# Kernel tuning notes

Measured on AMD Instinct MI355X. Metric: run time of the kernel, lower is better.

The kernel has to match this reference:

```python
import jax, jax.numpy as jnp
import numpy as np
from math import comb

B = 1024                 # num_batch
NUM, NVAR, NUM_OBS = 100, 11, 10
T_FIN = 15.0
K_P = 20.0; K_D = 2.0 * np.sqrt(20.0); K_P_V = 20.0
A_OBS, B_OBS = 8.0, 4.2
RHO_V, RHO_PROJ, RHO_LANE, RHO_OBS, RHO_OFFSET, RHO_INEQ = 1.0, 1.0, 100.0, 100.0, 1.0, 100.0
V_MIN, V_MAX, A_MAX = 0.1, 30.0, 8.0
MAXITER = 20
LATENT, HID, INP_DIM, TRAJ_DIM = 2, 1024, 55, 200


def _bernstein():
    # degree-10 Bernstein polynomial basis on [0, T_FIN], sampled at NUM points
    n = NVAR - 1
    s = np.linspace(0.0, 1.0, NUM)
    bm = lambda m: np.stack([comb(m, k) * s**k * (1.0 - s)**(m - k) for k in range(m + 1)], 1)
    P, B9, B8 = bm(n), bm(n - 1), bm(n - 2)
    Z = np.zeros(NUM)
    Pdot = np.stack([(n / T_FIN) * ((B9[:, k - 1] if k >= 1 else Z) - (B9[:, k] if k <= n - 1 else Z)) for k in range(n + 1)], 1)
    Pddot = np.stack([(n * (n - 1) / T_FIN**2) * ((B8[:, k - 2] if k >= 2 else Z) - 2.0 * (B8[:, k - 1] if 1 <= k <= n - 1 else Z) + (B8[:, k] if k <= n - 2 else Z)) for k in range(n + 1)], 1)
    return tuple(jnp.asarray(a, jnp.float32) for a in (P, Pdot, Pddot))


def _forward(inp, initial_state_ego, traj_gt, y_ub, y_lb, eps,
             enc_w1, enc_b1, enc_w2, enc_b2, enc_wmu, enc_bmu, enc_wlv, enc_blv,
             dec_w1, dec_b1, dec_w2, dec_b2, dec_w3, dec_b3,
             P, Pdot, Pddot, inp_mean, inp_std):
    Bn = inp.shape[0]
    tot_time = jnp.linspace(0.0, T_FIN, NUM)

    # ---- cVAE encode / reparameterize / decode ----
    inp_n = (inp - inp_mean) / inp_std
    h = jax.nn.relu(jnp.concatenate([inp_n, traj_gt], 1) @ enc_w1 + enc_b1)
    h = jax.nn.relu(h @ enc_w2 + enc_b2)
    mu = h @ enc_wmu + enc_bmu
    logvar = h @ enc_wlv + enc_blv
    z = mu + jnp.exp(0.5 * logvar) * eps
    h = jax.nn.relu(jnp.concatenate([z, inp_n], 1) @ dec_w1 + dec_b1)
    h = jax.nn.relu(h @ dec_w2 + dec_b2)
    nn_out = h @ dec_w3 + dec_b3          # (B, 8): 4 v_des + 4 y_des setpoints

    # ---- constant constraint matrices ----
    A_eq_x = jnp.stack([P[0], Pdot[0], Pddot[0]])                 # (3, 11)
    A_eq_y = jnp.stack([P[0], Pdot[0], Pddot[0], Pdot[-1]])       # (4, 11)
    A_pd = Pddot - K_P * P - K_D * Pdot
    A_vd = Pddot - K_P_V * Pdot
    cost_smooth = Pddot.T @ Pddot
    I = jnp.eye(NVAR, dtype=P.dtype)

    def kkt_inv(cost, A_eq):
        m = A_eq.shape[0]
        M = jnp.block([[cost, A_eq.T], [A_eq, jnp.zeros((m, m), cost.dtype)]])
        return jnp.linalg.inv(M)

    # ---- boundary conditions ----
    zb = jnp.zeros((Bn,), inp.dtype)
    b_eq_x = jnp.stack([zb, initial_state_ego[:, 2], zb], 1)
    b_eq_y = jnp.stack([zb, initial_state_ego[:, 3], zb, zb], 1)

    # ---- QP layer 1 (behavioral layer) ----
    # sum_i A_vd_i^T A_vd_i over the 4 row-partitions == A_vd^T A_vd
    cost1_x = cost_smooth + RHO_V * (A_vd.T @ A_vd)
    cost1_y = cost_smooth + RHO_OFFSET * (A_pd.T @ A_pd)
    inv1_x = kkt_inv(cost1_x, A_eq_x)
    inv1_y = kkt_inv(cost1_y, A_eq_y)
    v_des = jnp.repeat(nn_out[:, 0:4], NUM // 4, axis=1)   # (B, 100) piecewise setpoints
    y_des = jnp.repeat(nn_out[:, 4:8], NUM // 4, axis=1)
    lincost_x1 = -RHO_V * ((-K_P_V * v_des) @ A_vd)
    lincost_y1 = -RHO_OFFSET * ((-K_P * y_des) @ A_pd)
    c_x_bar = (jnp.concatenate([-lincost_x1, b_eq_x], 1) @ inv1_x.T)[:, :NVAR]
    c_y_bar = (jnp.concatenate([-lincost_y1, b_eq_y], 1) @ inv1_y.T)[:, :NVAR]

    # ---- obstacle constant-velocity rollouts (obstacle-major, matches tile(P)) ----
    x_obs, y_obs = inp[:, 5::5], inp[:, 6::5]
    vx_obs, vy_obs = inp[:, 7::5], inp[:, 8::5]
    x_obs_traj = (x_obs[:, :, None] + vx_obs[:, :, None] * tot_time).reshape(Bn, NUM_OBS * NUM)
    y_obs_traj = (y_obs[:, :, None] + vy_obs[:, :, None] * tot_time).reshape(Bn, NUM_OBS * NUM)

    # ---- QP layer 2 (iterative ADMM-style projection) ----
    A_obs_m = jnp.tile(P, (NUM_OBS, 1))          # (1000, 11)
    A_lane = jnp.vstack([P, -P])                 # (200, 11)
    A_vel, A_acc = Pdot, Pddot
    cost2_x = RHO_PROJ * I + RHO_OBS * (A_obs_m.T @ A_obs_m) + RHO_INEQ * (A_acc.T @ A_acc) + RHO_INEQ * (A_vel.T @ A_vel)
    cost2_y = cost2_x + RHO_LANE * (A_lane.T @ A_lane)
    inv2_x = kkt_inv(cost2_x, A_eq_x)
    inv2_y = kkt_inv(cost2_y, A_eq_y)
    ones_num = jnp.ones((1, NUM), inp.dtype)
    b_lane = jnp.concatenate([y_ub[:, None] * ones_num, -y_lb[:, None] * ones_num], 1)  # (B, 200)

    def step(carry, _):
        primal, lx, ly = carry
        cx, cy = primal[:, :NVAR], primal[:, NVAR:]
        x, xdot, xddot = cx @ P.T, cx @ Pdot.T, cx @ Pddot.T
        y, ydot, yddot = cy @ P.T, cy @ Pdot.T, cy @ Pddot.T
        # obstacle polar decomposition
        wc = jnp.tile(x, (1, NUM_OBS)) - x_obs_traj
        ws = jnp.tile(y, (1, NUM_OBS)) - y_obs_traj
        a_o = jnp.arctan2(A_OBS * ws, B_OBS * wc)
        ca, sa = jnp.cos(a_o), jnp.sin(a_o)
        c1 = RHO_OBS * (A_OBS**2 * ca**2 + B_OBS**2 * sa**2)
        c2 = RHO_OBS * (A_OBS * wc * ca + B_OBS * ws * sa)
        d_o = jnp.maximum(1.0, c2 / c1)
        # velocity / acceleration polar decomposition with box clipping
        a_v = jnp.arctan2(ydot, xdot)
        cv, sv = jnp.cos(a_v), jnp.sin(a_v)
        d_v = jnp.clip(xdot * cv + ydot * sv, V_MIN, V_MAX)
        a_a = jnp.arctan2(yddot, xddot)
        caa, saa = jnp.cos(a_a), jnp.sin(a_a)
        d_a = jnp.clip(xddot * caa + yddot * saa, 0.0, A_MAX)
        # lane slack
        lane_proj = cy @ A_lane.T
        s_lane = jnp.maximum(0.0, b_lane - lane_proj)
        res_lane = lane_proj - b_lane + s_lane
        # residuals -> dual updates
        rxo = wc - A_OBS * d_o * ca
        ryo = ws - B_OBS * d_o * sa
        rvx, rvy = xdot - d_v * cv, ydot - d_v * sv
        rax, ray = xddot - d_a * caa, yddot - d_a * saa
        lx = lx - RHO_OBS * (rxo @ A_obs_m) - RHO_INEQ * (rax @ A_acc) - RHO_INEQ * (rvx @ A_vel)
        ly = ly - RHO_OBS * (ryo @ A_obs_m) - RHO_INEQ * (ray @ A_acc) - RHO_INEQ * (rvy @ A_vel) - RHO_LANE * (res_lane @ A_lane)
        # linear cost + batched KKT solve via precomputed inverse
        b_ox = x_obs_traj + A_OBS * d_o * ca
        b_oy = y_obs_traj + B_OBS * d_o * sa
        lin_x = -lx - RHO_PROJ * c_x_bar - RHO_OBS * (b_ox @ A_obs_m) - RHO_INEQ * ((d_a * caa) @ A_acc) - RHO_INEQ * ((d_v * cv) @ A_vel)
        lin_y = -ly - RHO_PROJ * c_y_bar - RHO_OBS * (b_oy @ A_obs_m) - RHO_INEQ * ((d_a * saa) @ A_acc) - RHO_INEQ * ((d_v * sv) @ A_vel) - RHO_LANE * ((b_lane - s_lane) @ A_lane)
        sx = (jnp.concatenate([-lin_x, b_eq_x], 1) @ inv2_x.T)[:, :NVAR]
        sy = (jnp.concatenate([-lin_y, b_eq_y], 1) @ inv2_y.T)[:, :NVAR]
        return (jnp.concatenate([sx, sy], 1), lx, ly), None

    primal0 = jnp.concatenate([c_x_bar, c_y_bar], 1)
    lam0 = jnp.zeros((Bn, NVAR), inp.dtype)
    (primal, _, _), _ = jax.lax.scan(step, (primal0, lam0, lam0), None, length=MAXITER)
    return primal  # (B, 2*NVAR) projected trajectory coefficients


def setup_inputs() -> dict:
    key = jax.random.key(0)
    ks = jax.random.split(key, 16)
    P, Pdot, Pddot = _bernstein()
    n = lambda k, sh, sc=1.0: sc * jax.random.normal(k, sh, jnp.float32)
    return {
        "inp": n(ks[0], (B, INP_DIM), 5.0),
        "initial_state_ego": jnp.concatenate([jnp.zeros((B, 2), jnp.float32), 10.0 + n(ks[1], (B, 2))], 1),
        "traj_gt": n(ks[2], (B, TRAJ_DIM)),
        "y_ub": jnp.full((B,), 3.5, jnp.float32),
        "y_lb": jnp.full((B,), -3.5, jnp.float32),
        "eps": n(ks[3], (B, LATENT)),
        "enc_w1": n(ks[4], (INP_DIM + TRAJ_DIM, HID), 0.05), "enc_b1": jnp.zeros((HID,), jnp.float32),
        "enc_w2": n(ks[5], (HID, HID), 0.03), "enc_b2": jnp.zeros((HID,), jnp.float32),
        "enc_wmu": n(ks[6], (HID, LATENT), 0.03), "enc_bmu": jnp.zeros((LATENT,), jnp.float32),
        "enc_wlv": n(ks[7], (HID, LATENT), 0.03), "enc_blv": jnp.zeros((LATENT,), jnp.float32),
        "dec_w1": n(ks[8], (LATENT + INP_DIM, HID), 0.05), "dec_b1": jnp.zeros((HID,), jnp.float32),
        "dec_w2": n(ks[9], (HID, HID), 0.03), "dec_b2": jnp.zeros((HID,), jnp.float32),
        "dec_w3": n(ks[10], (HID, 8), 0.03), "dec_b3": jnp.zeros((8,), jnp.float32),
        "P": P, "Pdot": Pdot, "Pddot": Pddot,
        "inp_mean": jnp.zeros((INP_DIM,), jnp.float32),
        "inp_std": jnp.ones((INP_DIM,), jnp.float32),
    }


def reference(inp, initial_state_ego, traj_gt, y_ub, y_lb, eps,
              enc_w1, enc_b1, enc_w2, enc_b2, enc_wmu, enc_bmu, enc_wlv, enc_blv,
              dec_w1, dec_b1, dec_w2, dec_b2, dec_w3, dec_b3,
              P, Pdot, Pddot, inp_mean, inp_std):
    return _forward(inp, initial_state_ego, traj_gt, y_ub, y_lb, eps,
                    enc_w1, enc_b1, enc_w2, enc_b2, enc_wmu, enc_bmu, enc_wlv, enc_blv,
                    dec_w1, dec_b1, dec_w2, dec_b2, dec_w3, dec_b3,
                    P, Pdot, Pddot, inp_mean, inp_std)
```

## Files before the change

kernel.cpp:

```cpp
#include <hip/hip_runtime.h>
#include <hip/hip_bf16.h>
#include <math.h>

#define BATCH   1024
#define NUMPT   100
#define NVAR    11
#define NOBS    10
#define HID     1024
#define INPD    55
#define TRAJD   200

#define T_FIN_C   15.0f
#define K_P_C     20.0f
#define K_D_C     8.944271909999159f
#define K_P_V_C   20.0f
#define A_OBS_C   8.0f
#define B_OBS_C   4.2f
#define AB_C      33.6f
#define ABSQ_C    1128.96f
#define RHO_V_C      1.0f
#define RHO_PROJ_C   1.0f
#define RHO_LANE_C   100.0f
#define RHO_OBS_C    100.0f
#define RHO_OFFSET_C 1.0f
#define RHO_INEQ_C   100.0f
#define V_MIN_C   0.1f
#define V_MAX_C   30.0f
#define A_MAX_C   8.0f
#define MAXIT     20

#define WS_INV1X  0
#define WS_INV1Y  256
#define WS_INV2X  512
#define WS_INV2Y  768
#define WS_SVD    1024
#define WS_SPD    1088
#define WS_QX     1152
#define WS_QY     1280
#define WS_R2X    1408
#define WS_R2Y    1536
#define WS_BIG    2048

typedef __bf16 bf16x8 __attribute__((ext_vector_type(8)));
typedef float  f32x4  __attribute__((ext_vector_type(4)));

__global__ __launch_bounds__(256) void setup_kernel(
    const float* __restrict__ Pg, const float* __restrict__ Pdg,
    const float* __restrict__ Pddg, float* __restrict__ ws,
    const float* __restrict__ inp, const float* __restrict__ traj,
    const float* __restrict__ mean, const float* __restrict__ stdv,
    __bf16* __restrict__ enc_in, __bf16* __restrict__ dec_in,
    const float* __restrict__ w1, const float* __restrict__ w2,
    const float* __restrict__ w3, const float* __restrict__ w4,
    __bf16* __restrict__ o1, __bf16* __restrict__ o2,
    __bf16* __restrict__ o3, __bf16* __restrict__ o4)
{
    __shared__ float sP[NUMPT*NVAR], sPd[NUMPT*NVAR], sPdd[NUMPT*NVAR];
    __shared__ float aug[15][31];
    __shared__ float fcol[15];
    __shared__ float sQ[121];
    __shared__ float sn[INPD];
    __shared__ float tile[64][65];
    __shared__ float s_pivinv;
    __shared__ int   s_pidx;
    const int tid = threadIdx.x, bid = blockIdx.x;

    if (bid >= 1028) {
        const int tb = bid - 1028;
        int wsel, kt, nt;
        if (tb < 64)       { wsel = 0; kt = tb >> 4;        nt = tb & 15; }
        else if (tb < 320) { wsel = 1; kt = (tb-64) >> 4;   nt = (tb-64) & 15; }
        else if (tb < 352) { wsel = 2; kt = (tb-320) >> 4;  nt = (tb-320) & 15; }
        else               { wsel = 3; kt = (tb-352) >> 4;  nt = (tb-352) & 15; }
        const float* W = (wsel==0) ? w1 : (wsel==1) ? w2 : (wsel==2) ? w3 : w4;
        __bf16* O      = (wsel==0) ? o1 : (wsel==1) ? o2 : (wsel==2) ? o3 : o4;
        const int K  = (wsel==0) ? 255 : (wsel==2) ? 57 : 1024;
        const int Kp = (wsel==0) ? 256 : (wsel==2) ? 128 : 1024;
        if (kt*64 >= Kp) return;
        const int k0 = kt*64, n0 = nt*64;
        const int rr = tid >> 6, c = tid & 63;
        #pragma unroll 4
        for (int it = 0; it < 16; ++it) {
            const int r = it*4 + rr;
            tile[r][c] = (k0 + r < K) ? W[(size_t)(k0 + r)*HID + n0 + c] : 0.0f;
        }
        __syncthreads();
        #pragma unroll 4
        for (int it = 0; it < 16; ++it) {
            const int r = it*4 + rr;
            O[(size_t)(n0 + r)*Kp + k0 + c] = (__bf16)tile[c][r];
        }
        return;
    }

    if (bid >= 4) {
        const int b = bid - 4;
        if (tid < INPD) {
            const float v = (inp[b*INPD + tid] - mean[tid]) / stdv[tid];
            sn[tid] = v;
            enc_in[b*256 + tid] = (__bf16)v;
        } else if (tid < 255) {
            enc_in[b*256 + tid] = (__bf16)traj[b*TRAJD + (tid - INPD)];
        } else {
            enc_in[b*256 + 255] = (__bf16)0.0f;
        }
        __syncthreads();
        if (tid >= 2 && tid < 128)
            dec_in[b*128 + tid] = (__bf16)((tid < 57) ? sn[tid - 2] : 0.0f);
        return;
    }

    for (int i = tid; i < NUMPT*NVAR; i += 256) {
        sP[i] = Pg[i]; sPd[i] = Pdg[i]; sPdd[i] = Pddg[i];
    }
    for (int i = tid; i < 15*31; i += 256) (&aug[0][0])[i] = 0.0f;
    __syncthreads();

    const int N = (bid == 0 || bid == 2) ? 14 : 15;

    if (tid < 121) {
        const int i = tid / 11, j = tid % 11;
        float s = 0.0f;
        if (bid == 0) {
            for (int t = 0; t < NUMPT; ++t) {
                float pdd_i = sPdd[t*NVAR+i], pdd_j = sPdd[t*NVAR+j];
                float av_i = pdd_i - K_P_V_C * sPd[t*NVAR+i];
                float av_j = pdd_j - K_P_V_C * sPd[t*NVAR+j];
                s += pdd_i*pdd_j + RHO_V_C * av_i*av_j;
            }
        } else if (bid == 1) {
            for (int t = 0; t < NUMPT; ++t) {
                float pdd_i = sPdd[t*NVAR+i], pdd_j = sPdd[t*NVAR+j];
                float ap_i = pdd_i - K_P_C*sP[t*NVAR+i] - K_D_C*sPd[t*NVAR+i];
                float ap_j = pdd_j - K_P_C*sP[t*NVAR+j] - K_D_C*sPd[t*NVAR+j];
                s += pdd_i*pdd_j + RHO_OFFSET_C * ap_i*ap_j;
            }
        } else {
            float obs_w = RHO_OBS_C * (float)NOBS;
            if (bid == 3) obs_w += RHO_LANE_C * 2.0f;
            for (int t = 0; t < NUMPT; ++t) {
                float p_i = sP[t*NVAR+i],   p_j = sP[t*NVAR+j];
                float pd_i = sPd[t*NVAR+i], pd_j = sPd[t*NVAR+j];
                float pdd_i = sPdd[t*NVAR+i], pdd_j = sPdd[t*NVAR+j];
                s += obs_w*p_i*p_j + RHO_INEQ_C*(pdd_i*pdd_j + pd_i*pd_j);
            }
            if (i == j) s += RHO_PROJ_C;
        }
        aug[i][j] = s;
    }
    if (tid < 11) {
        const int i = tid;
        float a0 = sP[i], a1 = sPd[i], a2 = sPdd[i];
        aug[i][11] = a0; aug[11][i] = a0;
        aug[i][12] = a1; aug[12][i] = a1;
        aug[i][13] = a2; aug[13][i] = a2;
        if (N == 15) { float a3 = sPd[99*NVAR + i]; aug[i][14] = a3; aug[14][i] = a3; }
    }
    if (tid < N) aug[tid][N + tid] = 1.0f;

    if (bid == 0 && tid < 44) {
        const int c = tid / 11, k = tid % 11;
        float sv = 0.0f, sp = 0.0f;
        for (int t = 25*c; t < 25*c + 25; ++t) {
            float p = sP[t*NVAR+k], pd = sPd[t*NVAR+k], pdd = sPdd[t*NVAR+k];
            sv += pdd - K_P_V_C * pd;
            sp += pdd - K_P_C * p - K_D_C * pd;
        }
        ws[WS_SVD + tid] = sv;
        ws[WS_SPD + tid] = sp;
    }
    __syncthreads();

    if ((bid == 2 || bid == 3) && tid < 121) {
        float v = aug[tid/11][tid%11];
        if (tid/11 == tid%11) v -= RHO_PROJ_C;
        sQ[tid] = v;
        ws[(bid == 2 ? WS_QX : WS_QY) + tid] = v;
    }

    for (int k = 0; k < N; ++k) {
        if (tid == 0) {
            int p = k; float best = fabsf(aug[k][k]);
            for (int i = k+1; i < N; ++i) {
                float v = fabsf(aug[i][k]);
                if (v > best) { best = v; p = i; }
            }
            s_pidx = p;
        }
        __syncthreads();
        const int p = s_pidx;
        if (p != k && tid < 2*N) {
            float tmp = aug[k][tid]; aug[k][tid] = aug[p][tid]; aug[p][tid] = tmp;
        }
        __syncthreads();
        if (tid == 0) s_pivinv = 1.0f / aug[k][k];
        __syncthreads();
        if (tid < 2*N) aug[k][tid] *= s_pivinv;
        __syncthreads();
        if (tid < N) fcol[tid] = (tid == k) ? 0.0f : aug[tid][k];
        __syncthreads();
        for (int idx = tid; idx < N*2*N; idx += 256) {
            const int i = idx / (2*N), j = idx % (2*N);
            if (i != k) aug[i][j] = fmaf(-fcol[i], aug[k][j], aug[i][j]);
        }
        __syncthreads();
    }

    float* dst = ws + (bid == 0 ? WS_INV1X : bid == 1 ? WS_INV1Y
                      : bid == 2 ? WS_INV2X : WS_INV2Y);
    for (int idx = tid; idx < N*N; idx += 256)
        dst[idx] = aug[idx / N][N + idx % N];
    __syncthreads();

    if ((bid == 2 || bid == 3) && tid < 121) {
        const int k = tid / 11, j = tid % 11;
        float a = 0.0f;
        #pragma unroll
        for (int m = 0; m < 11; ++m) a = fmaf(aug[k][N + m], sQ[m*11 + j], a);
        ws[(bid == 2 ? WS_R2X : WS_R2Y) + tid] = a;
    }
}

#define GEMM_CORE(A_, Wt_, Kp_, ...)                                          \
    __shared__ __bf16 As[2][32][136];                                         \
    __shared__ __bf16 Bs[2][64][136];                                         \
    const int lane = tid & 63, wv = tid >> 6;                                 \
    const int wm = (wv >> 1) * 16, wn = (wv & 1) * 32;                        \
    const int ln = lane & 15, q = lane >> 4;                                  \
    const int row0 = blockIdx.y * 32, col0 = blockIdx.x * 64;                 \
    const int r16 = tid >> 4, ch = (tid & 15) * 8;                            \
    f32x4 acc0 = (f32x4){0,0,0,0}, acc1 = (f32x4){0,0,0,0};                   \
    {                                                                         \
        bf16x8 va = *(const bf16x8*)&(A_)[(size_t)(row0 + r16)*(Kp_) + ch];   \
        bf16x8 vb = *(const bf16x8*)&(A_)[(size_t)(row0 + r16 + 16)*(Kp_) + ch]; \
        __VA_ARGS__                                                           \
        *(bf16x8*)&As[0][r16][ch] = va;                                       \
        *(bf16x8*)&As[0][r16 + 16][ch] = vb;                                  \
        _Pragma("unroll")                                                     \
        for (int p = 0; p < 4; ++p)                                           \
            *(bf16x8*)&Bs[0][r16 + 16*p][ch] =                                \
                *(const bf16x8*)&(Wt_)[(size_t)(col0 + r16 + 16*p)*(Kp_) + ch]; \
    }                                                                         \
    __syncthreads();                                                          \
    int cur = 0;                                                              \
    for (int k0 = 128; k0 < (Kp_); k0 += 128) {                               \
        const bf16x8 nva = *(const bf16x8*)&(A_)[(size_t)(row0 + r16)*(Kp_) + k0 + ch]; \
        const bf16x8 nvb = *(const bf16x8*)&(A_)[(size_t)(row0 + r16 + 16)*(Kp_) + k0 + ch]; \
        const bf16x8 nw0 = *(const bf16x8*)&(Wt_)[(size_t)(col0 + r16)*(Kp_) + k0 + ch]; \
        const bf16x8 nw1 = *(const bf16x8*)&(Wt_)[(size_t)(col0 + r16 + 16)*(Kp_) + k0 + ch]; \
        const bf16x8 nw2 = *(const bf16x8*)&(Wt_)[(size_t)(col0 + r16 + 32)*(Kp_) + k0 + ch]; \
        const bf16x8 nw3 = *(const bf16x8*)&(Wt_)[(size_t)(col0 + r16 + 48)*(Kp_) + k0 + ch]; \
        _Pragma("unroll")                                                     \
        for (int kc = 0; kc < 4; ++kc) {                                      \
            const bf16x8 a  = *(const bf16x8*)&As[cur][wm + ln][kc*32 + q*8]; \
            const bf16x8 b0 = *(const bf16x8*)&Bs[cur][wn + ln][kc*32 + q*8]; \
            const bf16x8 b1 = *(const bf16x8*)&Bs[cur][wn + 16 + ln][kc*32 + q*8]; \
            acc0 = __builtin_amdgcn_mfma_f32_16x16x32_bf16(a, b0, acc0, 0, 0, 0); \
            acc1 = __builtin_amdgcn_mfma_f32_16x16x32_bf16(a, b1, acc1, 0, 0, 0); \
        }                                                                     \
        const int nxt = cur ^ 1;                                              \
        *(bf16x8*)&As[nxt][r16][ch] = nva;                                    \
        *(bf16x8*)&As[nxt][r16 + 16][ch] = nvb;                               \
        *(bf16x8*)&Bs[nxt][r16][ch] = nw0;                                    \
        *(bf16x8*)&Bs[nxt][r16 + 16][ch] = nw1;                               \
        *(bf16x8*)&Bs[nxt][r16 + 32][ch] = nw2;                               \
        *(bf16x8*)&Bs[nxt][r16 + 48][ch] = nw3;                               \
        __syncthreads();                                                      \
        cur = nxt;                                                            \
    }                                                                         \
    _Pragma("unroll")                                                         \
    for (int kc = 0; kc < 4; ++kc) {                                          \
        const bf16x8 a  = *(const bf16x8*)&As[cur][wm + ln][kc*32 + q*8];     \
        const bf16x8 b0 = *(const bf16x8*)&Bs[cur][wn + ln][kc*32 + q*8];     \
        const bf16x8 b1 = *(const bf16x8*)&Bs[cur][wn + 16 + ln][kc*32 + q*8]; \
        acc0 = __builtin_amdgcn_mfma_f32_16x16x32_bf16(a, b0, acc0, 0, 0, 0); \
        acc1 = __builtin_amdgcn_mfma_f32_16x16x32_bf16(a, b1, acc1, 0, 0, 0); \
    }

#define GEMM_WRITE_RELU(C_)                                                   \
    _Pragma("unroll")                                                         \
    for (int ni = 0; ni < 2; ++ni) {                                          \
        const int col = col0 + wn + ni*16 + ln;                               \
        const float bv = bias[col];                                           \
        const f32x4 av = ni ? acc1 : acc0;                                    \
        _Pragma("unroll")                                                     \
        for (int r = 0; r < 4; ++r) {                                         \
            const int row = row0 + wm + q*4 + r;                              \
            (C_)[(size_t)row * HID + col] = (__bf16)fmaxf(av[r] + bv, 0.0f);  \
        }                                                                     \
    }

__global__ __launch_bounds__(256) void gemm_relu(
    const __bf16* __restrict__ A, const __bf16* __restrict__ Wt,
    const float* __restrict__ bias, __bf16* __restrict__ C, int Kp)
{
    const int tid = threadIdx.x;
    GEMM_CORE(A, Wt, Kp)
    GEMM_WRITE_RELU(C)
}

__global__ __launch_bounds__(256) void gemm_mulv(
    const __bf16* __restrict__ A, const __bf16* __restrict__ Wt,
    const float* __restrict__ bias,
    const float* __restrict__ wmu, const float* __restrict__ wlv,
    float* __restrict__ pmulv, int Kp)
{
    const int tid = threadIdx.x;
    GEMM_CORE(A, Wt, Kp)
    const int c0 = col0 + wn + ln;
    const int c1 = c0 + 16;
    const float b0v = bias[c0], b1v = bias[c1];
    const float wm00 = wmu[c0*2+0], wm01 = wmu[c0*2+1];
    const float wm10 = wmu[c1*2+0], wm11 = wmu[c1*2+1];
    const float wl00 = wlv[c0*2+0], wl01 = wlv[c0*2+1];
    const float wl10 = wlv[c1*2+0], wl11 = wlv[c1*2+1];
    float pr[4][4];
    #pragma unroll
    for (int r = 0; r < 4; ++r) {
        const float h0 = fmaxf(acc0[r] + b0v, 0.0f);
        const float h1 = fmaxf(acc1[r] + b1v, 0.0f);
        pr[r][0] = fmaf(h0, wm00, h1*wm10);
        pr[r][1] = fmaf(h0, wm01, h1*wm11);
        pr[r][2] = fmaf(h0, wl00, h1*wl10);
        pr[r][3] = fmaf(h0, wl01, h1*wl11);
    }
    #pragma unroll
    for (int m = 1; m <= 8; m <<= 1)
        #pragma unroll
        for (int r = 0; r < 4; ++r)
            #pragma unroll
            for (int j = 0; j < 4; ++j)
                pr[r][j] += __shfl_xor(pr[r][j], m);
    if (ln == 0) {
        const int part = blockIdx.x*2 + (wv & 1);
        #pragma unroll
        for (int r = 0; r < 4; ++r) {
            const int row = row0 + wm + q*4 + r;
            *(float4*)&pmulv[(size_t)row*128 + part*4] =
                make_float4(pr[r][0], pr[r][1], pr[r][2], pr[r][3]);
        }
    }
}

__global__ __launch_bounds__(256) void gemm_zfix(
    const __bf16* __restrict__ A, const __bf16* __restrict__ Wt,
    const float* __restrict__ bias, __bf16* __restrict__ C, int Kp,
    const float* __restrict__ pmulv, const float* __restrict__ bmu,
    const float* __restrict__ blv, const float* __restrict__ eps)
{
    __shared__ float zsh[32][2];
    const int tid = threadIdx.x;
    {
        const int row = tid >> 3, pg = tid & 7;
        const int ra = blockIdx.y*32 + row;
        float4 s = make_float4(0.0f, 0.0f, 0.0f, 0.0f);
        #pragma unroll
        for (int p = pg*4; p < pg*4 + 4; ++p) {
            const float4 qa = *(const float4*)&pmulv[(size_t)ra*128 + p*4];
            s.x += qa.x; s.y += qa.y; s.z += qa.z; s.w += qa.w;
        }
        #pragma unroll
        for (int m = 1; m <= 4; m <<= 1) {
            s.x += __shfl_down(s.x, m);
            s.y += __shfl_down(s.y, m);
            s.z += __shfl_down(s.z, m);
            s.w += __shfl_down(s.w, m);
        }
        if (pg == 0) {
            zsh[row][0] = fmaf(expf(0.5f*(s.z + blv[0])), eps[ra*2+0], s.x + bmu[0]);
            zsh[row][1] = fmaf(expf(0.5f*(s.w + blv[1])), eps[ra*2+1], s.y + bmu[1]);
        }
    }
    __syncthreads();
    GEMM_CORE(A, Wt, Kp,
        if (ch == 0) {
            va[0] = (__bf16)zsh[r16][0];
            va[1] = (__bf16)zsh[r16][1];
            vb[0] = (__bf16)zsh[r16 + 16][0];
            vb[1] = (__bf16)zsh[r16 + 16][1];
        }
    )
    GEMM_WRITE_RELU(C)
}

__global__ __launch_bounds__(256) void gemm_out8(
    const __bf16* __restrict__ A, const __bf16* __restrict__ Wt,
    const float* __restrict__ bias, const float* __restrict__ w3,
    float* __restrict__ pnn, int Kp)
{
    const int tid = threadIdx.x;
    GEMM_CORE(A, Wt, Kp)
    const int c0 = col0 + wn + ln;
    const int c1 = c0 + 16;
    const float b0v = bias[c0], b1v = bias[c1];
    float pr[4][8];
    #pragma unroll
    for (int r = 0; r < 4; ++r) {
        const float h0 = fmaxf(acc0[r] + b0v, 0.0f);
        const float h1 = fmaxf(acc1[r] + b1v, 0.0f);
        #pragma unroll
        for (int j = 0; j < 8; ++j)
            pr[r][j] = fmaf(h0, w3[c0*8 + j], h1*w3[c1*8 + j]);
    }
    #pragma unroll
    for (int m = 1; m <= 8; m <<= 1)
        #pragma unroll
        for (int r = 0; r < 4; ++r)
            #pragma unroll
            for (int j = 0; j < 8; ++j)
                pr[r][j] += __shfl_xor(pr[r][j], m);
    if (ln == 0) {
        const int part = blockIdx.x*2 + (wv & 1);
        #pragma unroll
        for (int r = 0; r < 4; ++r) {
            const int row = row0 + wm + q*4 + r;
            *(float4*)&pnn[(size_t)row*256 + part*8] =
                make_float4(pr[r][0], pr[r][1], pr[r][2], pr[r][3]);
            *(float4*)&pnn[(size_t)row*256 + part*8 + 4] =
                make_float4(pr[r][4], pr[r][5], pr[r][6], pr[r][7]);
        }
    }
}

#define DOT11(bb, a0, a1, a2) \
    fmaf(bb[0],a0.x, fmaf(bb[1],a0.y, fmaf(bb[2],a0.z, fmaf(bb[3],a0.w, \
    fmaf(bb[4],a1.x, fmaf(bb[5],a1.y, fmaf(bb[6],a1.z, fmaf(bb[7],a1.w, \
    fmaf(bb[8],a2.x, fmaf(bb[9],a2.y, bb[10]*a2.z))))))))))

__global__ __launch_bounds__(256) void solver_kernel(
    const float* __restrict__ pnn, const float* __restrict__ b3,
    const float* __restrict__ inp,
    const float* __restrict__ ise, const float* __restrict__ yub_p,
    const float* __restrict__ ylb_p,
    const float* __restrict__ Pg, const float* __restrict__ Pdg,
    const float* __restrict__ Pddg,
    const float* __restrict__ ws, float* __restrict__ out)
{
    __shared__ __align__(16) float sBcol[3][11][108];
    __shared__ float s_i2x[196], s_i2y[225], sR2x[121], sR2y[121];
    __shared__ __align__(16) float rows[7][104];
    __shared__ float dval[2][80];
    __shared__ __align__(16) float cxs[12], cys[12];
    __shared__ float wlin[24];
    __shared__ float obsS[4][10];
    __shared__ float nnS[8];

    const int tid = threadIdx.x;
    const int e = blockIdx.x;

    for (int i = tid; i < 3*11*108; i += 256) {
        const int mat = i / 1188, rem = i - mat*1188;
        const int k = rem / 108, t = rem - k*108;
        const float* G = (mat == 0) ? Pg : (mat == 1 ? Pdg : Pddg);
        sBcol[mat][k][t] = (t < NUMPT) ? G[t*NVAR + k] : 0.0f;
    }
    for (int i = tid; i < 196; i += 256) s_i2x[i] = ws[WS_INV2X + i];
    for (int i = tid; i < 225; i += 256) s_i2y[i] = ws[WS_INV2Y + i];
    for (int i = tid; i < 121; i += 256) { sR2x[i] = ws[WS_R2X + i]; sR2y[i] = ws[WS_R2Y + i]; }
    if (tid >= 112 && tid < 152) {
        const int i = tid - 112;
        obsS[i/10][i%10] = inp[e*INPD + 5 + (i/10) + 5*(i%10)];
    }
    if (tid >= 192) {
        const int l = tid - 192;
        const int j = l & 7, pg = l >> 3;
        float s = 0.0f;
        #pragma unroll
        for (int p = pg*4; p < pg*4 + 4; ++p)
            s += pnn[(size_t)e*256 + p*8 + j];
        s += __shfl_down(s, 8);
        s += __shfl_down(s, 16);
        s += __shfl_down(s, 32);
        if (pg == 0) nnS[j] = b3[j] + s;
    }
    if (tid >= 64 && tid < 92) {
        const int i = tid - 64;
        rows[i >> 2][100 + (i & 3)] = 0.0f;
    }
    if (tid == 92) cxs[11] = 0.0f;
    if (tid == 93) cys[11] = 0.0f;

    const bool isA = (tid < 200);
    const int tA = tid >> 1, hA2 = tid & 1;
    const bool isB = (tid < 154);
    const int hB = (tid >= 77) ? 1 : 0;
    const int dB = tid - 77*hB;
    const int rB = dB / 11, kB = dB - 11*rB;
    const int mB = (rB==1||rB==4) ? 2 : ((rB==2||rB==5) ? 1 : 0);
    const float* colp = &sBcol[mB][kB][hB*52];
    const float* rowp = &rows[rB][hB*52];

    float bP[NVAR], bQ[NVAR];
    if (isA) {
        const float* Qsrc = hA2 ? Pddg : Pdg;
        #pragma unroll
        for (int k = 0; k < NVAR; ++k) {
            bP[k] = Pg[tA*NVAR+k];
            bQ[k] = Qsrc[tA*NVAR+k];
        }
    }

    const float vx0 = ise[e*4 + 2], vy0 = ise[e*4 + 3];
    const float yub = yub_p[e], ylb = ylb_p[e];
    __syncthreads();

    const float DT = T_FIN_C / 99.0f;
    float xo[5], yo[5];
    if (isA) {
        const int ob0 = 5*hA2;
        #pragma unroll
        for (int o = 0; o < 5; ++o) {
            xo[o] = fmaf(obsS[2][ob0+o], tA*DT, obsS[0][ob0+o]);
            yo[o] = fmaf(obsS[3][ob0+o], tA*DT, obsS[1][ob0+o]);
        }
    }

    if (tid < 11) {
        float s = 0;
        #pragma unroll
        for (int c = 0; c < 4; ++c)
            s = fmaf(nnS[c], ws[WS_SVD + c*11 + tid], s);
        wlin[tid] = RHO_V_C * K_P_V_C * s;
    } else if (tid < 22) {
        const int k = tid - 11;
        float s = 0;
        #pragma unroll
        for (int c = 0; c < 4; ++c)
            s = fmaf(nnS[4 + c], ws[WS_SPD + c*11 + k], s);
        wlin[tid] = RHO_OFFSET_C * K_P_C * s;
    }
    __syncthreads();

    float lam = 0.0f, cb = 0.0f;
    if (tid < 11) {
        const int k = tid;
        float a = vx0 * ws[WS_INV1X + k*14 + 12];
        #pragma unroll
        for (int j = 0; j < NVAR; ++j)
            a = fmaf(-wlin[j], ws[WS_INV1X + k*14 + j], a);
        cb = a; cxs[k] = a;
    } else if (tid < 22) {
        const int k = tid - 11;
        float a = vy0 * ws[WS_INV1Y + k*15 + 12];
        #pragma unroll
        for (int j = 0; j < NVAR; ++j)
            a = fmaf(-wlin[11 + j], ws[WS_INV1Y + k*15 + j], a);
        cb = a; cys[k] = a;
    }
    __syncthreads();

    for (int it = 0; it < MAXIT; ++it) {
        if (isA) {
            const float4 x0 = *(const float4*)&cxs[0];
            const float4 x1 = *(const float4*)&cxs[4];
            const float4 x2 = *(const float4*)&cxs[8];
            const float4 y0 = *(const float4*)&cys[0];
            const float4 y1 = *(const float4*)&cys[4];
            const float4 y2 = *(const float4*)&cys[8];
            const float px = DOT11(bP, x0, x1, x2);
            const float py = DOT11(bP, y0, y1, y2);
            const float qx = DOT11(bQ, x0, x1, x2);
            const float qy = DOT11(bQ, y0, y1, y2);

            float srx = 0.0f, sry = 0.0f;
            #pragma unroll
            for (int o = 0; o < 5; ++o) {
                const float wc = px - xo[o], wsv = py - yo[o];
                const float aw = A_OBS_C * wsv, bw = B_OBS_C * wc;
                const float r2 = aw*aw + bw*bw;
                if (r2 > 0.0f) {
                    const float f = (r2 < ABSQ_C) ? (1.0f - AB_C * rsqrtf(r2)) : 0.0f;
                    srx = fmaf(wc, f, srx);
                    sry = fmaf(wsv, f, sry);
                } else {
                    srx -= A_OBS_C;
                }
            }
            const float mrx = srx + __shfl_xor(srx, 1);
            const float mry = sry + __shfl_xor(sry, 1);

            if (hA2 == 0) {
                rows[0][tA] = mrx;
                rows[3][tA] = mry;
                const float rv2 = qx*qx + qy*qy;
                float vxr, vyr;
                if (rv2 > 0.0f) {
                    const float ri = rsqrtf(rv2);
                    const float dv = fminf(fmaxf(rv2*ri, V_MIN_C), V_MAX_C);
                    const float f = 1.0f - dv*ri;
                    vxr = qx*f; vyr = qy*f;
                } else { vxr = -V_MIN_C; vyr = 0.0f; }
                rows[2][tA] = vxr;  rows[5][tA] = vyr;
                rows[6][tA] = fmaxf(0.0f, py - yub) - fmaxf(0.0f, ylb - py);
            } else {
                const float ra2 = qx*qx + qy*qy;
                float axr = 0.0f, ayr = 0.0f;
                if (ra2 > A_MAX_C*A_MAX_C) {
                    const float ri = rsqrtf(ra2);
                    const float f = 1.0f - A_MAX_C*ri;
                    axr = qx*f; ayr = qy*f;
                }
                rows[1][tA] = axr;  rows[4][tA] = ayr;
            }
        }
        __syncthreads();

        if (isB) {
            float s0 = 0.0f, s1 = 0.0f;
            #pragma unroll
            for (int i = 0; i < 13; ++i) {
                const float4 rr = *(const float4*)&rowp[i*4];
                const float4 cc = *(const float4*)&colp[i*4];
                s0 = fmaf(rr.x, cc.x, s0); s1 = fmaf(rr.y, cc.y, s1);
                s0 = fmaf(rr.z, cc.z, s0); s1 = fmaf(rr.w, cc.w, s1);
            }
            dval[hB][dB] = s0 + s1;
        }
        __syncthreads();

        if (tid < 22) {
            const int k = (tid < 11) ? tid : tid - 11;
            float u;
            if (tid < 11)
                u = RHO_OBS_C * ((dval[0][k]      + dval[1][k])
                               + (dval[0][11 + k] + dval[1][11 + k])
                               + (dval[0][22 + k] + dval[1][22 + k]));
            else
                u = RHO_OBS_C * ((dval[0][33 + k] + dval[1][33 + k])
                               + (dval[0][44 + k] + dval[1][44 + k])
                               + (dval[0][55 + k] + dval[1][55 + k])
                               + (dval[0][66 + k] + dval[1][66 + k]));
            wlin[tid] = 2.0f*u - lam - cb;
            lam -= u;
        }
        __builtin_amdgcn_wave_barrier();
        if (tid < 22) {
            const int k = (tid < 11) ? tid : tid - 11;
            if (tid < 11) {
                float a = vx0 * s_i2x[k*14 + 12];
                #pragma unroll
                for (int j = 0; j < NVAR; ++j) {
                    a = fmaf(-wlin[j], s_i2x[k*14 + j], a);
                    a = fmaf(sR2x[k*11 + j], cxs[j], a);
                }
                cxs[k] = a;
            } else {
                float a = vy0 * s_i2y[k*15 + 12];
                #pragma unroll
                for (int j = 0; j < NVAR; ++j) {
                    a = fmaf(-wlin[11 + j], s_i2y[k*15 + j], a);
                    a = fmaf(sR2y[k*11 + j], cys[j], a);
                }
                cys[k] = a;
            }
        }
        __syncthreads();
    }

    if (tid < NVAR) {
        out[e*22 + tid]      = cxs[tid];
        out[e*22 + 11 + tid] = cys[tid];
    }
}

extern "C" void kernel_launch(void* const* d_in, const int* in_sizes, int n_in,
                              void* d_out, int out_size, void* d_ws, size_t ws_size,
                              hipStream_t stream)
{
    (void)in_sizes; (void)n_in; (void)out_size; (void)ws_size;
    const float* inp    = (const float*)d_in[0];
    const float* ise    = (const float*)d_in[1];
    const float* traj   = (const float*)d_in[2];
    const float* yub    = (const float*)d_in[3];
    const float* ylb    = (const float*)d_in[4];
    const float* eps    = (const float*)d_in[5];
    const float* enc_w1 = (const float*)d_in[6];
    const float* enc_b1 = (const float*)d_in[7];
    const float* enc_w2 = (const float*)d_in[8];
    const float* enc_b2 = (const float*)d_in[9];
    const float* wmu    = (const float*)d_in[10];
    const float* bmu    = (const float*)d_in[11];
    const float* wlv    = (const float*)d_in[12];
    const float* blv    = (const float*)d_in[13];
    const float* dec_w1 = (const float*)d_in[14];
    const float* dec_b1 = (const float*)d_in[15];
    const float* dec_w2 = (const float*)d_in[16];
    const float* dec_b2 = (const float*)d_in[17];
    const float* dec_w3 = (const float*)d_in[18];
    const float* dec_b3 = (const float*)d_in[19];
    const float* P      = (const float*)d_in[20];
    const float* Pd     = (const float*)d_in[21];
    const float* Pdd    = (const float*)d_in[22];
    const float* mean   = (const float*)d_in[23];
    const float* stdv   = (const float*)d_in[24];

    float* ws    = (float*)d_ws;
    float* pmulv = ws + WS_BIG;
    float* pnn   = pmulv + (size_t)BATCH*128;
    __bf16* bfb  = (__bf16*)(pnn + (size_t)BATCH*256);
    __bf16* enc_in = bfb;
    __bf16* dec_in = enc_in + (size_t)BATCH*256;
    __bf16* hA     = dec_in + (size_t)BATCH*128;
    __bf16* wt1    = hA + (size_t)BATCH*HID;
    __bf16* wt2    = wt1 + (size_t)HID*256;
    __bf16* wt3    = wt2 + (size_t)HID*HID;
    __bf16* wt4    = wt3 + (size_t)HID*128;
    float* outf = (float*)d_out;

    setup_kernel<<<4 + 1024 + 608, 256, 0, stream>>>(
        P, Pd, Pdd, ws, inp, traj, mean, stdv, enc_in, dec_in,
        enc_w1, enc_w2, dec_w1, dec_w2, wt1, wt2, wt3, wt4);

    dim3 g(16, 32);
    gemm_relu<<<g, 256, 0, stream>>>(enc_in, wt1, enc_b1, hA, 256);
    gemm_mulv<<<g, 256, 0, stream>>>(hA, wt2, enc_b2, wmu, wlv, pmulv, 1024);
    gemm_zfix<<<g, 256, 0, stream>>>(dec_in, wt3, dec_b1, hA, 128,
                                     pmulv, bmu, blv, eps);
    gemm_out8<<<g, 256, 0, stream>>>(hA, wt4, dec_b2, dec_w3, pnn, 1024);
    solver_kernel<<<BATCH, 256, 0, stream>>>(pnn, dec_b3, inp, ise, yub, ylb,
                                             P, Pd, Pdd, ws, outf);
}
```

Before: 215.1 us.

## Retile MLP GEMMs to 64x64 output tiles with 512 threads and 64-wide K steps

Changes the shared GEMM core from 32x64 output tiles with 256 threads and 128-wide K chunks to 64x64 tiles with 8 waves and 64-wide K chunks. Each block now reuses every loaded weight row across twice as many activation rows, halving redundant weight traffic, and the grid shrinks from 512 to 256 blocks. The trade-off is fewer blocks to spread across CUs, twice as many barrier iterations along K, and less MFMA work between syncs. Epilogue partial-index math and the z-injection in the decoder GEMM are adjusted to the new wave layout.

```diff
diff --git a/kernel.cpp b/kernel.cpp
--- a/kernel.cpp
+++ b/kernel.cpp
@@ -222,36 +222,28 @@
 }
 
 #define GEMM_CORE(A_, Wt_, Kp_, ...)                                          \
-    __shared__ __bf16 As[2][32][136];                                         \
-    __shared__ __bf16 Bs[2][64][136];                                         \
+    __shared__ __bf16 As[2][64][72];                                          \
+    __shared__ __bf16 Bs[2][64][72];                                          \
     const int lane = tid & 63, wv = tid >> 6;                                 \
-    const int wm = (wv >> 1) * 16, wn = (wv & 1) * 32;                        \
+    const int wm = (wv & 3) * 16, wn = (wv >> 2) * 32;                        \
     const int ln = lane & 15, q = lane >> 4;                                  \
-    const int row0 = blockIdx.y * 32, col0 = blockIdx.x * 64;                 \
-    const int r16 = tid >> 4, ch = (tid & 15) * 8;                            \
+    const int row0 = blockIdx.y * 64, col0 = blockIdx.x * 64;                 \
+    const int lrow = tid >> 3, lc8 = (tid & 7) * 8;                           \
     f32x4 acc0 = (f32x4){0,0,0,0}, acc1 = (f32x4){0,0,0,0};                   \
     {                                                                         \
-        bf16x8 va = *(const bf16x8*)&(A_)[(size_t)(row0 + r16)*(Kp_) + ch];   \
-        bf16x8 vb = *(const bf16x8*)&(A_)[(size_t)(row0 + r16 + 16)*(Kp_) + ch]; \
+        bf16x8 va = *(const bf16x8*)&(A_)[(size_t)(row0 + lrow)*(Kp_) + lc8]; \
         __VA_ARGS__                                                           \
-        *(bf16x8*)&As[0][r16][ch] = va;                                       \
-        *(bf16x8*)&As[0][r16 + 16][ch] = vb;                                  \
-        _Pragma("unroll")                                                     \
-        for (int p = 0; p < 4; ++p)                                           \
-            *(bf16x8*)&Bs[0][r16 + 16*p][ch] =                                \
-                *(const bf16x8*)&(Wt_)[(size_t)(col0 + r16 + 16*p)*(Kp_) + ch]; \
+        *(bf16x8*)&As[0][lrow][lc8] = va;                                     \
+        *(bf16x8*)&Bs[0][lrow][lc8] =                                         \
+            *(const bf16x8*)&(Wt_)[(size_t)(col0 + lrow)*(Kp_) + lc8];        \
     }                                                                         \
     __syncthreads();                                                          \
     int cur = 0;                                                              \
-    for (int k0 = 128; k0 < (Kp_); k0 += 128) {                               \
-        const bf16x8 nva = *(const bf16x8*)&(A_)[(size_t)(row0 + r16)*(Kp_) + k0 + ch]; \
-        const bf16x8 nvb = *(const bf16x8*)&(A_)[(size_t)(row0 + r16 + 16)*(Kp_) + k0 + ch]; \
-        const bf16x8 nw0 = *(const bf16x8*)&(Wt_)[(size_t)(col0 + r16)*(Kp_) + k0 + ch]; \
-        const bf16x8 nw1 = *(const bf16x8*)&(Wt_)[(size_t)(col0 + r16 + 16)*(Kp_) + k0 + ch]; \
-        const bf16x8 nw2 = *(const bf16x8*)&(Wt_)[(size_t)(col0 + r16 + 32)*(Kp_) + k0 + ch]; \
-        const bf16x8 nw3 = *(const bf16x8*)&(Wt_)[(size_t)(col0 + r16 + 48)*(Kp_) + k0 + ch]; \
+    for (int k0 = 64; k0 < (Kp_); k0 += 64) {                                 \
+        const bf16x8 nva = *(const bf16x8*)&(A_)[(size_t)(row0 + lrow)*(Kp_) + k0 + lc8]; \
+        const bf16x8 nwb = *(const bf16x8*)&(Wt_)[(size_t)(col0 + lrow)*(Kp_) + k0 + lc8]; \
         _Pragma("unroll")                                                     \
-        for (int kc = 0; kc < 4; ++kc) {                                      \
+        for (int kc = 0; kc < 2; ++kc) {                                      \
             const bf16x8 a  = *(const bf16x8*)&As[cur][wm + ln][kc*32 + q*8]; \
             const bf16x8 b0 = *(const bf16x8*)&Bs[cur][wn + ln][kc*32 + q*8]; \
             const bf16x8 b1 = *(const bf16x8*)&Bs[cur][wn + 16 + ln][kc*32 + q*8]; \
@@ -259,17 +251,13 @@
             acc1 = __builtin_amdgcn_mfma_f32_16x16x32_bf16(a, b1, acc1, 0, 0, 0); \
         }                                                                     \
         const int nxt = cur ^ 1;                                              \
-        *(bf16x8*)&As[nxt][r16][ch] = nva;                                    \
-        *(bf16x8*)&As[nxt][r16 + 16][ch] = nvb;                               \
-        *(bf16x8*)&Bs[nxt][r16][ch] = nw0;                                    \
-        *(bf16x8*)&Bs[nxt][r16 + 16][ch] = nw1;                               \
-        *(bf16x8*)&Bs[nxt][r16 + 32][ch] = nw2;                               \
-        *(bf16x8*)&Bs[nxt][r16 + 48][ch] = nw3;                               \
+        *(bf16x8*)&As[nxt][lrow][lc8] = nva;                                  \
+        *(bf16x8*)&Bs[nxt][lrow][lc8] = nwb;                                  \
         __syncthreads();                                                      \
         cur = nxt;                                                            \
     }                                                                         \
     _Pragma("unroll")                                                         \
-    for (int kc = 0; kc < 4; ++kc) {                                          \
+    for (int kc = 0; kc < 2; ++kc) {                                          \
         const bf16x8 a  = *(const bf16x8*)&As[cur][wm + ln][kc*32 + q*8];     \
         const bf16x8 b0 = *(const bf16x8*)&Bs[cur][wn + ln][kc*32 + q*8];     \
         const bf16x8 b1 = *(const bf16x8*)&Bs[cur][wn + 16 + ln][kc*32 + q*8]; \
@@ -290,7 +278,7 @@
         }                                                                     \
     }
 
-__global__ __launch_bounds__(256) void gemm_relu(
+__global__ __launch_bounds__(512) void gemm_relu(
     const __bf16* __restrict__ A, const __bf16* __restrict__ Wt,
     const float* __restrict__ bias, __bf16* __restrict__ C, int Kp)
 {
@@ -299,7 +287,7 @@
     GEMM_WRITE_RELU(C)
 }
 
-__global__ __launch_bounds__(256) void gemm_mulv(
+__global__ __launch_bounds__(512) void gemm_mulv(
     const __bf16* __restrict__ A, const __bf16* __restrict__ Wt,
     const float* __restrict__ bias,
     const float* __restrict__ wmu, const float* __restrict__ wlv,
@@ -332,7 +320,7 @@
             for (int j = 0; j < 4; ++j)
                 pr[r][j] += __shfl_xor(pr[r][j], m);
     if (ln == 0) {
-        const int part = blockIdx.x*2 + (wv & 1);
+        const int part = blockIdx.x*2 + (wv >> 2);
         #pragma unroll
         for (int r = 0; r < 4; ++r) {
             const int row = row0 + wm + q*4 + r;
@@ -342,17 +330,17 @@
     }
 }
 
-__global__ __launch_bounds__(256) void gemm_zfix(
+__global__ __launch_bounds__(512) void gemm_zfix(
     const __bf16* __restrict__ A, const __bf16* __restrict__ Wt,
     const float* __restrict__ bias, __bf16* __restrict__ C, int Kp,
     const float* __restrict__ pmulv, const float* __restrict__ bmu,
     const float* __restrict__ blv, const float* __restrict__ eps)
 {
-    __shared__ float zsh[32][2];
+    __shared__ float zsh[64][2];
     const int tid = threadIdx.x;
     {
         const int row = tid >> 3, pg = tid & 7;
-        const int ra = blockIdx.y*32 + row;
+        const int ra = blockIdx.y*64 + row;
         float4 s = make_float4(0.0f, 0.0f, 0.0f, 0.0f);
         #pragma unroll
         for (int p = pg*4; p < pg*4 + 4; ++p) {
@@ -373,17 +361,15 @@
     }
     __syncthreads();
     GEMM_CORE(A, Wt, Kp,
-        if (ch == 0) {
-            va[0] = (__bf16)zsh[r16][0];
-            va[1] = (__bf16)zsh[r16][1];
-            vb[0] = (__bf16)zsh[r16 + 16][0];
-            vb[1] = (__bf16)zsh[r16 + 16][1];
+        if (lc8 == 0) {
+            va[0] = (__bf16)zsh[lrow][0];
+            va[1] = (__bf16)zsh[lrow][1];
         }
     )
     GEMM_WRITE_RELU(C)
 }
 
-__global__ __launch_bounds__(256) void gemm_out8(
+__global__ __launch_bounds__(512) void gemm_out8(
     const __bf16* __restrict__ A, const __bf16* __restrict__ Wt,
     const float* __restrict__ bias, const float* __restrict__ w3,
     float* __restrict__ pnn, int Kp)
@@ -410,7 +396,7 @@
             for (int j = 0; j < 8; ++j)
                 pr[r][j] += __shfl_xor(pr[r][j], m);
     if (ln == 0) {
-        const int part = blockIdx.x*2 + (wv & 1);
+        const int part = blockIdx.x*2 + (wv >> 2);
         #pragma unroll
         for (int r = 0; r < 4; ++r) {
             const int row = row0 + wm + q*4 + r;
@@ -711,12 +697,12 @@
         P, Pd, Pdd, ws, inp, traj, mean, stdv, enc_in, dec_in,
         enc_w1, enc_w2, dec_w1, dec_w2, wt1, wt2, wt3, wt4);
 
-    dim3 g(16, 32);
-    gemm_relu<<<g, 256, 0, stream>>>(enc_in, wt1, enc_b1, hA, 256);
-    gemm_mulv<<<g, 256, 0, stream>>>(hA, wt2, enc_b2, wmu, wlv, pmulv, 1024);
-    gemm_zfix<<<g, 256, 0, stream>>>(dec_in, wt3, dec_b1, hA, 128,
+    dim3 g(16, 16);
+    gemm_relu<<<g, 512, 0, stream>>>(enc_in, wt1, enc_b1, hA, 256);
+    gemm_mulv<<<g, 512, 0, stream>>>(hA, wt2, enc_b2, wmu, wlv, pmulv, 1024);
+    gemm_zfix<<<g, 512, 0, stream>>>(dec_in, wt3, dec_b1, hA, 128,
                                      pmulv, bmu, blv, eps);
-    gemm_out8<<<g, 256, 0, stream>>>(hA, wt4, dec_b2, dec_w3, pnn, 1024);
+    gemm_out8<<<g, 512, 0, stream>>>(hA, wt4, dec_b2, dec_w3, pnn, 1024);
     solver_kernel<<<BATCH, 256, 0, stream>>>(pnn, dec_b3, inp, ise, yub, ylb,
                                              P, Pd, Pdd, ws, outf);
 }
```

Measured after the change: 218.1 us. Within noise of the previous version (+1.4%).

## Compute four KKT inversions per-wavefront in one block with wave-level sync

Applied to the files above, without the earlier changes.

The four small KKT matrix inversions move from four separate blocks into a single block, one wavefront per matrix. Block-wide __syncthreads are replaced by wave barriers, and the serial pivot search becomes a shuffle reduction. This cuts the barrier and serial-thread latency of the Gauss-Jordan elimination in the setup kernel. The cost is less parallelism per matrix (64 lanes instead of 256) and a larger shared-memory footprint.

```diff
diff --git a/kernel.cpp b/kernel.cpp
--- a/kernel.cpp
+++ b/kernel.cpp
@@ -56,13 +56,11 @@
     __bf16* __restrict__ o3, __bf16* __restrict__ o4)
 {
     __shared__ float sP[NUMPT*NVAR], sPd[NUMPT*NVAR], sPdd[NUMPT*NVAR];
-    __shared__ float aug[15][31];
-    __shared__ float fcol[15];
-    __shared__ float sQ[121];
+    __shared__ float aug4[4][15][31];
+    __shared__ float fcolW[4][16];
+    __shared__ float sQw[2][121];
     __shared__ float sn[INPD];
     __shared__ float tile[64][65];
-    __shared__ float s_pivinv;
-    __shared__ int   s_pidx;
     const int tid = threadIdx.x, bid = blockIdx.x;
 
     if (bid >= 1028) {
@@ -110,25 +108,30 @@
         return;
     }
 
+    if (bid != 0) return;
+
+    const int w = tid >> 6, lane = tid & 63;
+    const int N = (w == 0 || w == 2) ? 14 : 15;
+
     for (int i = tid; i < NUMPT*NVAR; i += 256) {
         sP[i] = Pg[i]; sPd[i] = Pdg[i]; sPdd[i] = Pddg[i];
     }
-    for (int i = tid; i < 15*31; i += 256) (&aug[0][0])[i] = 0.0f;
     __syncthreads();
 
-    const int N = (bid == 0 || bid == 2) ? 14 : 15;
-
-    if (tid < 121) {
-        const int i = tid / 11, j = tid % 11;
+    for (int e = lane; e < 465; e += 64) ((float*)aug4[w])[e] = 0.0f;
+    __builtin_amdgcn_wave_barrier();
+
+    for (int e = lane; e < 121; e += 64) {
+        const int i = e / 11, j = e % 11;
         float s = 0.0f;
-        if (bid == 0) {
+        if (w == 0) {
             for (int t = 0; t < NUMPT; ++t) {
                 float pdd_i = sPdd[t*NVAR+i], pdd_j = sPdd[t*NVAR+j];
                 float av_i = pdd_i - K_P_V_C * sPd[t*NVAR+i];
                 float av_j = pdd_j - K_P_V_C * sPd[t*NVAR+j];
                 s += pdd_i*pdd_j + RHO_V_C * av_i*av_j;
             }
-        } else if (bid == 1) {
+        } else if (w == 1) {
             for (int t = 0; t < NUMPT; ++t) {
                 float pdd_i = sPdd[t*NVAR+i], pdd_j = sPdd[t*NVAR+j];
                 float ap_i = pdd_i - K_P_C*sP[t*NVAR+i] - K_D_C*sPd[t*NVAR+i];
@@ -137,7 +140,7 @@
             }
         } else {
             float obs_w = RHO_OBS_C * (float)NOBS;
-            if (bid == 3) obs_w += RHO_LANE_C * 2.0f;
+            if (w == 3) obs_w += RHO_LANE_C * 2.0f;
             for (int t = 0; t < NUMPT; ++t) {
                 float p_i = sP[t*NVAR+i],   p_j = sP[t*NVAR+j];
                 float pd_i = sPd[t*NVAR+i], pd_j = sPd[t*NVAR+j];
@@ -146,78 +149,87 @@
             }
             if (i == j) s += RHO_PROJ_C;
         }
-        aug[i][j] = s;
-    }
-    if (tid < 11) {
-        const int i = tid;
-        float a0 = sP[i], a1 = sPd[i], a2 = sPdd[i];
-        aug[i][11] = a0; aug[11][i] = a0;
-        aug[i][12] = a1; aug[12][i] = a1;
-        aug[i][13] = a2; aug[13][i] = a2;
-        if (N == 15) { float a3 = sPd[99*NVAR + i]; aug[i][14] = a3; aug[14][i] = a3; }
-    }
-    if (tid < N) aug[tid][N + tid] = 1.0f;
-
-    if (bid == 0 && tid < 44) {
-        const int c = tid / 11, k = tid % 11;
+        aug4[w][i][j] = s;
+    }
+    if (lane < 11) {
+        const int i = lane;
+        const float a0 = sP[i], a1 = sPd[i], a2 = sPdd[i];
+        aug4[w][i][11] = a0; aug4[w][11][i] = a0;
+        aug4[w][i][12] = a1; aug4[w][12][i] = a1;
+        aug4[w][i][13] = a2; aug4[w][13][i] = a2;
+        if (N == 15) {
+            const float a3 = sPd[99*NVAR + i];
+            aug4[w][i][14] = a3; aug4[w][14][i] = a3;
+        }
+    }
+    if (lane < N) aug4[w][lane][N + lane] = 1.0f;
+
+    if (w == 0 && lane < 44) {
+        const int c = lane / 11, k = lane % 11;
         float sv = 0.0f, sp = 0.0f;
         for (int t = 25*c; t < 25*c + 25; ++t) {
             float p = sP[t*NVAR+k], pd = sPd[t*NVAR+k], pdd = sPdd[t*NVAR+k];
             sv += pdd - K_P_V_C * pd;
             sp += pdd - K_P_C * p - K_D_C * pd;
         }
-        ws[WS_SVD + tid] = sv;
-        ws[WS_SPD + tid] = sp;
-    }
-    __syncthreads();
-
-    if ((bid == 2 || bid == 3) && tid < 121) {
-        float v = aug[tid/11][tid%11];
-        if (tid/11 == tid%11) v -= RHO_PROJ_C;
-        sQ[tid] = v;
-        ws[(bid == 2 ? WS_QX : WS_QY) + tid] = v;
-    }
+        ws[WS_SVD + lane] = sv;
+        ws[WS_SPD + lane] = sp;
+    }
+    __builtin_amdgcn_wave_barrier();
+
+    if (w >= 2) {
+        for (int e = lane; e < 121; e += 64) {
+            float v = aug4[w][e/11][e%11];
+            if (e/11 == e%11) v -= RHO_PROJ_C;
+            sQw[w-2][e] = v;
+            ws[(w == 2 ? WS_QX : WS_QY) + e] = v;
+        }
+    }
+    __builtin_amdgcn_wave_barrier();
 
     for (int k = 0; k < N; ++k) {
-        if (tid == 0) {
-            int p = k; float best = fabsf(aug[k][k]);
-            for (int i = k+1; i < N; ++i) {
-                float v = fabsf(aug[i][k]);
-                if (v > best) { best = v; p = i; }
-            }
-            s_pidx = p;
-        }
-        __syncthreads();
-        const int p = s_pidx;
-        if (p != k && tid < 2*N) {
-            float tmp = aug[k][tid]; aug[k][tid] = aug[p][tid]; aug[p][tid] = tmp;
-        }
-        __syncthreads();
-        if (tid == 0) s_pivinv = 1.0f / aug[k][k];
-        __syncthreads();
-        if (tid < 2*N) aug[k][tid] *= s_pivinv;
-        __syncthreads();
-        if (tid < N) fcol[tid] = (tid == k) ? 0.0f : aug[tid][k];
-        __syncthreads();
-        for (int idx = tid; idx < N*2*N; idx += 256) {
-            const int i = idx / (2*N), j = idx % (2*N);
-            if (i != k) aug[i][j] = fmaf(-fcol[i], aug[k][j], aug[i][j]);
-        }
-        __syncthreads();
-    }
-
-    float* dst = ws + (bid == 0 ? WS_INV1X : bid == 1 ? WS_INV1Y
-                      : bid == 2 ? WS_INV2X : WS_INV2Y);
-    for (int idx = tid; idx < N*N; idx += 256)
-        dst[idx] = aug[idx / N][N + idx % N];
-    __syncthreads();
-
-    if ((bid == 2 || bid == 3) && tid < 121) {
-        const int k = tid / 11, j = tid % 11;
-        float a = 0.0f;
-        #pragma unroll
-        for (int m = 0; m < 11; ++m) a = fmaf(aug[k][N + m], sQ[m*11 + j], a);
-        ws[(bid == 2 ? WS_R2X : WS_R2Y) + tid] = a;
+        float pv = (lane < N && lane >= k) ? fabsf(aug4[w][lane][k]) : -1.0f;
+        int   pi = lane;
+        #pragma unroll
+        for (int m = 1; m <= 8; m <<= 1) {
+            const float ov = __shfl_xor(pv, m);
+            const int   oi = __shfl_xor(pi, m);
+            if (ov > pv) { pv = ov; pi = oi; }
+        }
+        const int p = __shfl(pi, 0);
+        if (p != k && lane < 2*N) {
+            const float tmp = aug4[w][k][lane];
+            aug4[w][k][lane] = aug4[w][p][lane];
+            aug4[w][p][lane] = tmp;
+        }
+        __builtin_amdgcn_wave_barrier();
+        const float inv = 1.0f / aug4[w][k][k];
+        if (lane < 2*N) aug4[w][k][lane] *= inv;
+        if (lane < N) fcolW[w][lane] = (lane == k) ? 0.0f : aug4[w][lane][k];
+        __builtin_amdgcn_wave_barrier();
+        for (int e = lane; e < N*2*N; e += 64) {
+            const int i = e / (2*N), j = e - i*(2*N);
+            if (i != k)
+                aug4[w][i][j] = fmaf(-fcolW[w][i], aug4[w][k][j], aug4[w][i][j]);
+        }
+        __builtin_amdgcn_wave_barrier();
+    }
+
+    float* dst = ws + (w == 0 ? WS_INV1X : w == 1 ? WS_INV1Y
+                      : w == 2 ? WS_INV2X : WS_INV2Y);
+    for (int e = lane; e < N*N; e += 64)
+        dst[e] = aug4[w][e / N][N + e % N];
+    __builtin_amdgcn_wave_barrier();
+
+    if (w >= 2) {
+        for (int e = lane; e < 121; e += 64) {
+            const int k = e / 11, j = e % 11;
+            float a = 0.0f;
+            #pragma unroll
+            for (int m = 0; m < 11; ++m)
+                a = fmaf(aug4[w][k][N + m], sQw[w-2][m*11 + j], a);
+            ws[(w == 2 ? WS_R2X : WS_R2Y) + e] = a;
+        }
     }
 }
 
```

Result: slower. 227.8 us (+5.9%).
